# Kernel tuning notes

Measured on AMD Instinct MI355X. Metric: run time of the kernel, lower is better.

Reference implementation:

```python
import jax, jax.numpy as jnp
import numpy as np

N, L, H, D = 8, 1024, 16, 64
HD = H * D          # hidden_size = 1024
MLP = 4 * HD        # mlp_dim = 4096
EPS = 1e-5


def _layer_norm(x, g, b):
    mu = jnp.mean(x, axis=-1, keepdims=True)
    var = jnp.var(x, axis=-1, keepdims=True)
    return (x - mu) * jax.lax.rsqrt(var + EPS) * g + b


def setup_inputs() -> dict:
    key = jax.random.key(0)
    ks = jax.random.split(key, 8)
    s_in = 1.0 / np.sqrt(HD)
    s_mlp = 1.0 / np.sqrt(MLP)
    return {
        "x": jax.random.normal(ks[0], (N, L, HD), jnp.float32),
        "ln0_g": jnp.ones((HD,), jnp.float32),
        "ln0_b": jnp.zeros((HD,), jnp.float32),
        "wq": jax.random.normal(ks[1], (HD, HD), jnp.float32) * s_in,
        "bq": jnp.zeros((HD,), jnp.float32),
        "wk": jax.random.normal(ks[2], (HD, HD), jnp.float32) * s_in,
        "bk": jnp.zeros((HD,), jnp.float32),
        "wv": jax.random.normal(ks[3], (HD, HD), jnp.float32) * s_in,
        "bv": jnp.zeros((HD,), jnp.float32),
        "wo": jax.random.normal(ks[4], (HD, HD), jnp.float32) * s_in,
        "bo": jnp.zeros((HD,), jnp.float32),
        "ln1_g": jnp.ones((HD,), jnp.float32),
        "ln1_b": jnp.zeros((HD,), jnp.float32),
        "w1": jax.random.normal(ks[5], (HD, MLP), jnp.float32) * s_in,
        "b1": jnp.zeros((MLP,), jnp.float32),
        "w2": jax.random.normal(ks[6], (MLP, HD), jnp.float32) * s_mlp,
        "b2": jnp.zeros((HD,), jnp.float32),
    }


def reference(x, ln0_g, ln0_b, wq, bq, wk, bk, wv, bv, wo, bo,
              ln1_g, ln1_b, w1, b1, w2, b2):
    n, l, hd = x.shape
    # --- pre-LN self-attention ---
    y = _layer_norm(x, ln0_g, ln0_b)
    q = (y @ wq + bq).reshape(n, l, H, D)
    k = (y @ wk + bk).reshape(n, l, H, D)
    v = (y @ wv + bv).reshape(n, l, H, D)
    qkt = jnp.einsum('nqhd,nkhd->nqkh', q, k) / jnp.sqrt(jnp.float32(D))
    attn = jax.nn.softmax(qkt, axis=2)
    y = jnp.einsum('nqkh,nkhd->nqhd', attn, v).reshape(n, l, hd)
    y = y @ wo + bo
    x = x + y  # residual (dropout_rate=0 in eval)
    # --- pre-LN MLP ---
    y = _layer_norm(x, ln1_g, ln1_b)
    y = jax.nn.gelu(y @ w1 + b1)
    y = y @ w2 + b2
    return x + y
```

## Files before the change

kernel.cpp:

```cpp
#include <hip/hip_runtime.h>
#include <math.h>

typedef __attribute__((ext_vector_type(8))) __bf16 bf16x8;
typedef __attribute__((ext_vector_type(4))) float f32x4;

#define NBATCH 8
#define SEQ    1024
#define NHEAD  16
#define DHEAD  64
#define HID    1024
#define MLPD   4096

static __device__ __forceinline__ unsigned short f2bf(float f) {
  unsigned int u = __float_as_uint(f);
  u += 0x7fffu + ((u >> 16) & 1u);
  return (unsigned short)(u >> 16);
}

static __device__ __forceinline__ void gload_lds16(const unsigned short* g,
                                                   unsigned short* l) {
  __builtin_amdgcn_global_load_lds(
      (const __attribute__((address_space(1))) unsigned int*)g,
      (__attribute__((address_space(3))) unsigned int*)l, 16, 0, 0);
}

static __device__ __forceinline__ float gelu_fast(float v) {
  const float z = 0.7978845608028654f * (v + 0.044715f * v * v * v);
  const float e = __expf(-2.0f * fabsf(z));
  float th = (1.0f - e) / (1.0f + e);
  th = copysignf(th, z);
  return 0.5f * v * (1.0f + th);
}

__global__ __launch_bounds__(256) void k_transpose(const float* __restrict__ in,
                                                   unsigned short* __restrict__ out,
                                                   int R, int C) {
  __shared__ float t[32][33];
  const int tx = threadIdx.x & 31, ty = threadIdx.x >> 5;
  const int c0 = blockIdx.x * 32, r0 = blockIdx.y * 32;
#pragma unroll
  for (int j = 0; j < 4; ++j)
    t[ty + j * 8][tx] = in[(size_t)(r0 + ty + j * 8) * C + c0 + tx];
  __syncthreads();
#pragma unroll
  for (int j = 0; j < 4; ++j)
    out[(size_t)(c0 + ty + j * 8) * R + r0 + tx] = f2bf(t[tx][ty + j * 8]);
}

__global__ void k_pack_bias(const float* __restrict__ bq, const float* __restrict__ bk,
                            const float* __restrict__ bv, float* __restrict__ o) {
  int i = blockIdx.x * 256 + threadIdx.x;
  if (i < 3 * HID) {
    float v = (i < HID) ? bq[i] : (i < 2 * HID ? bk[i - HID] : bv[i - 2 * HID]);
    o[i] = v;
  }
}

__global__ __launch_bounds__(256) void k_ln(const float* __restrict__ x,
                                            const float* __restrict__ gw,
                                            const float* __restrict__ bw,
                                            unsigned short* __restrict__ y) {
  __shared__ float red[2][4];
  const int row = blockIdx.x;
  const int tid = threadIdx.x;
  const float4 v = ((const float4*)(x + (size_t)row * HID))[tid];
  float sum = v.x + v.y + v.z + v.w;
  float sq  = v.x * v.x + v.y * v.y + v.z * v.z + v.w * v.w;
#pragma unroll
  for (int off = 32; off >= 1; off >>= 1) {
    sum += __shfl_xor(sum, off);
    sq  += __shfl_xor(sq, off);
  }
  if ((tid & 63) == 0) { red[0][tid >> 6] = sum; red[1][tid >> 6] = sq; }
  __syncthreads();
  sum = red[0][0] + red[0][1] + red[0][2] + red[0][3];
  sq  = red[1][0] + red[1][1] + red[1][2] + red[1][3];
  const float mu  = sum * (1.0f / HID);
  const float var = sq * (1.0f / HID) - mu * mu;
  const float rs  = rsqrtf(var + 1e-5f);
  const float4 g4 = ((const float4*)gw)[tid];
  const float4 b4 = ((const float4*)bw)[tid];
  ushort4 ov;
  ov.x = f2bf((v.x - mu) * rs * g4.x + b4.x);
  ov.y = f2bf((v.y - mu) * rs * g4.y + b4.y);
  ov.z = f2bf((v.z - mu) * rs * g4.z + b4.z);
  ov.w = f2bf((v.w - mu) * rs * g4.w + b4.w);
  ((ushort4*)(y + (size_t)row * HID))[tid] = ov;
}

template <int EPI, int BN>
__global__ __launch_bounds__(512, 2) void k_gemm(const unsigned short* __restrict__ A,
                                                 const unsigned short* __restrict__ BT,
                                                 const float* __restrict__ bias,
                                                 const float* __restrict__ res,
                                                 void* __restrict__ Cout,
                                                 int M, int N, int K) {
  constexpr int ASZ = 256 * 64;
  constexpr int BSZ = BN * 64;
  constexpr int NF  = BN / 64;
  constexpr int NCW = BN / 4;
  constexpr int BCALLS = BN / 64;
  __shared__ unsigned short sh[2 * ASZ + 2 * BSZ];

  const int tid  = threadIdx.x;
  const int lane = tid & 63;
  const int w    = tid >> 6;
  const int wr   = w >> 2, wc = w & 3;
  const int l15  = lane & 15, g = lane >> 4;
  const int m0 = blockIdx.y * 256, n0 = blockIdx.x * BN;

  f32x4 acc[8][NF] = {};

  const int srow  = w * 8 + (lane >> 3);
  const int scolb = ((lane & 7) * 16) ^ (((lane >> 3) & 7) << 4);
  const unsigned short* pA = A  + (size_t)(m0 + srow) * K + (scolb >> 1);
  const unsigned short* pB = BT + (size_t)(n0 + srow) * K + (scolb >> 1);
  unsigned short* shB = sh + 2 * ASZ;

#define STAGE(buf, kk)                                                          \
  do {                                                                          \
    _Pragma("unroll") for (int c = 0; c < 4; ++c)                               \
      gload_lds16(pA + (size_t)c * 64 * K + (kk),                               \
                  sh + (buf) * ASZ + (c * 64 + w * 8) * 64);                    \
    _Pragma("unroll") for (int c = 0; c < BCALLS; ++c)                          \
      gload_lds16(pB + (size_t)c * 64 * K + (kk),                               \
                  shB + (buf) * BSZ + (c * 64 + w * 8) * 64);                   \
  } while (0)

  const int fmask = (l15 & 7) << 4;
  const int bo0 = ((0 * 64) + g * 16) ^ fmask;
  const int bo1 = ((1 * 64) + g * 16) ^ fmask;
  const int aRowBase = wr * 128 + l15;
  const int bRowBase = wc * NCW + l15;

  const int NT = K >> 6;

  STAGE(0, 0);
  int buf = 0;
  for (int t = 0; t < NT; ++t) {
    asm volatile("s_waitcnt vmcnt(0)" ::: "memory");
    __builtin_amdgcn_sched_barrier(0);
    __builtin_amdgcn_s_barrier();
    if (t + 1 < NT) STAGE(buf ^ 1, (t + 1) * 64);

    const unsigned short* shAb = sh + buf * ASZ;
    const unsigned short* shBb = shB + buf * BSZ;

    bf16x8 bfr[NF][2];
#pragma unroll
    for (int n = 0; n < NF; ++n) {
      const int br = (bRowBase + n * 16) * 64;
      bfr[n][0] = *(const bf16x8*)(shBb + br + (bo0 >> 1));
      bfr[n][1] = *(const bf16x8*)(shBb + br + (bo1 >> 1));
    }

#pragma unroll
    for (int p = 0; p < 4; ++p) {
      const int ar0 = (aRowBase + (2 * p) * 16) * 64;
      const int ar1 = (aRowBase + (2 * p + 1) * 16) * 64;
      const bf16x8 a00 = *(const bf16x8*)(shAb + ar0 + (bo0 >> 1));
      const bf16x8 a01 = *(const bf16x8*)(shAb + ar0 + (bo1 >> 1));
      const bf16x8 a10 = *(const bf16x8*)(shAb + ar1 + (bo0 >> 1));
      const bf16x8 a11 = *(const bf16x8*)(shAb + ar1 + (bo1 >> 1));
      __builtin_amdgcn_s_barrier();
      asm volatile("s_waitcnt lgkmcnt(0)" ::: "memory");
      __builtin_amdgcn_sched_barrier(0);
      __builtin_amdgcn_s_setprio(1);
#pragma unroll
      for (int n = 0; n < NF; ++n) {
        acc[2 * p][n]     = __builtin_amdgcn_mfma_f32_16x16x32_bf16(a00, bfr[n][0], acc[2 * p][n], 0, 0, 0);
        acc[2 * p][n]     = __builtin_amdgcn_mfma_f32_16x16x32_bf16(a01, bfr[n][1], acc[2 * p][n], 0, 0, 0);
        acc[2 * p + 1][n] = __builtin_amdgcn_mfma_f32_16x16x32_bf16(a10, bfr[n][0], acc[2 * p + 1][n], 0, 0, 0);
        acc[2 * p + 1][n] = __builtin_amdgcn_mfma_f32_16x16x32_bf16(a11, bfr[n][1], acc[2 * p + 1][n], 0, 0, 0);
      }
      __builtin_amdgcn_s_setprio(0);
      __builtin_amdgcn_s_barrier();
    }
    buf ^= 1;
  }
#undef STAGE

  if constexpr (EPI == 2) {
#pragma unroll
    for (int m = 0; m < 8; ++m) {
#pragma unroll
      for (int n = 0; n < NF; ++n) {
        const int col = n0 + wc * NCW + n * 16 + l15;
        const float bc = bias[col];
#pragma unroll
        for (int r = 0; r < 4; ++r) {
          const int row = m0 + wr * 128 + m * 16 + g * 4 + r;
          const size_t idx = (size_t)row * N + col;
          ((float*)Cout)[idx] = acc[m][n][r] + bc + res[idx];
        }
      }
    }
  } else {
    unsigned short* ep = sh + w * (128 * NCW);
#pragma unroll
    for (int m = 0; m < 8; ++m) {
#pragma unroll
      for (int n = 0; n < NF; ++n) {
        const float bc = bias[n0 + wc * NCW + n * 16 + l15];
#pragma unroll
        for (int r = 0; r < 4; ++r) {
          float v = acc[m][n][r] + bc;
          if constexpr (EPI == 1) v = gelu_fast(v);
          ep[(m * 16 + g * 4 + r) * NCW + n * 16 + l15] = f2bf(v);
        }
      }
    }
    constexpr int CPR = NCW / 8;
#pragma unroll
    for (int j = 0; j < NCW / 4; ++j) {
      const int t = lane + j * 64;
      const int row = t / CPR, colb = (t % CPR) * 8;
      const uint4 vv = *(const uint4*)(ep + row * NCW + colb);
      unsigned short* outp = (unsigned short*)Cout +
          (size_t)(m0 + wr * 128 + row) * N + n0 + wc * NCW + colb;
      *(uint4*)outp = vv;
    }
  }
}

__global__ __launch_bounds__(256) void k_vt(const unsigned short* __restrict__ qkv,
                                            unsigned short* __restrict__ vT) {
  __shared__ unsigned short t[64][72];
  const int nh = blockIdx.y;
  const int nb = nh >> 4, h = nh & 15;
  const int l0 = blockIdx.x * 64;
  const int tx = threadIdx.x & 7;
  const int ty = threadIdx.x >> 3;
  const unsigned short* src = qkv + (size_t)(nb * SEQ + l0) * 3072 + 2048 + h * DHEAD;
#pragma unroll
  for (int j = 0; j < 2; ++j)
    *(uint4*)(&t[ty + j * 32][tx * 8]) =
        *(const uint4*)(&src[(size_t)(ty + j * 32) * 3072 + tx * 8]);
  __syncthreads();
  unsigned short* dst = vT + (size_t)nh * DHEAD * SEQ + l0;
#pragma unroll
  for (int j = 0; j < 2; ++j) {
    const int d = ty + j * 32;
    ushort4 a, b;
    a.x = t[tx * 8 + 0][d]; a.y = t[tx * 8 + 1][d];
    a.z = t[tx * 8 + 2][d]; a.w = t[tx * 8 + 3][d];
    b.x = t[tx * 8 + 4][d]; b.y = t[tx * 8 + 5][d];
    b.z = t[tx * 8 + 6][d]; b.w = t[tx * 8 + 7][d];
    *(ushort4*)(&dst[(size_t)d * SEQ + tx * 8])     = a;
    *(ushort4*)(&dst[(size_t)d * SEQ + tx * 8 + 4]) = b;
  }
}

#define SOFTMAX_GROUP(S, gq)                                                       \
  {                                                                                \
    float mx = -INFINITY;                                                          \
    _Pragma("unroll") for (int c = 0; c < 4; ++c)                                  \
      _Pragma("unroll") for (int r = 0; r < 4; ++r)                                \
        mx = fmaxf(mx, S[c][r]);                                                   \
    mx = fmaxf(mx, __shfl_xor(mx, 16));                                            \
    mx = fmaxf(mx, __shfl_xor(mx, 32));                                            \
    const float mnew = fmaxf(m_run[gq], mx);                                       \
    const float sc = __expf(0.125f * (m_run[gq] - mnew));                          \
    m_run[gq] = mnew;                                                              \
    float ts = 0.0f;                                                               \
    _Pragma("unroll") for (int c = 0; c < 4; ++c) {                                \
      const float p0 = __expf(0.125f * (S[c][0] - mnew));                          \
      const float p1 = __expf(0.125f * (S[c][1] - mnew));                          \
      const float p2 = __expf(0.125f * (S[c][2] - mnew));                          \
      const float p3 = __expf(0.125f * (S[c][3] - mnew));                          \
      ts += (p0 + p1) + (p2 + p3);                                                 \
      const unsigned int lo = (unsigned int)f2bf(p0) | ((unsigned int)f2bf(p1) << 16); \
      const unsigned int hi = (unsigned int)f2bf(p2) | ((unsigned int)f2bf(p3) << 16); \
      *(uint2*)(&P_lds[w][((gq) * 16 + l15) * 72 + c * 16 + g * 4]) = make_uint2(lo, hi); \
    }                                                                              \
    ts += __shfl_xor(ts, 16);                                                      \
    ts += __shfl_xor(ts, 32);                                                      \
    s_run[gq] = s_run[gq] * sc + ts;                                               \
    const float scr0 = __shfl(sc, g * 4 + 0), scr1 = __shfl(sc, g * 4 + 1);        \
    const float scr2 = __shfl(sc, g * 4 + 2), scr3 = __shfl(sc, g * 4 + 3);        \
    _Pragma("unroll") for (int dt = 0; dt < 4; ++dt) {                             \
      o[gq][dt][0] *= scr0; o[gq][dt][1] *= scr1;                                  \
      o[gq][dt][2] *= scr2; o[gq][dt][3] *= scr3;                                  \
    }                                                                              \
  }

__global__ __launch_bounds__(256, 4) void k_attn(const unsigned short* __restrict__ qkv,
                                                 const unsigned short* __restrict__ vT,
                                                 unsigned short* __restrict__ outp) {
  __shared__ unsigned short Ks[64 * 64];
  __shared__ unsigned short Vs[64 * 64];
  __shared__ unsigned short P_lds[4][32 * 72];
  const int tid  = threadIdx.x;
  const int lane = tid & 63;
  const int w    = tid >> 6;
  const int l15  = lane & 15, g = lane >> 4;
  const int nh = blockIdx.y;
  const int nb = nh >> 4, h = nh & 15;
  const int q0 = blockIdx.x * 128 + w * 32;
  const size_t RS = 3 * HID;

  const unsigned short* Qp = qkv + (size_t)(nb * SEQ + q0) * RS + h * DHEAD;
  const unsigned short* Kg = qkv + (size_t)(nb * SEQ) * RS + HID + h * DHEAD;
  const unsigned short* Vg = vT + (size_t)nh * DHEAD * SEQ;

  const int L0 = tid * 32, L1 = L0 + 16;
  const int kr0 = L0 >> 7, kc0 = (L0 & 127) ^ ((kr0 & 7) << 4);
  const int kr1 = L1 >> 7, kc1 = (L1 & 127) ^ ((kr1 & 7) << 4);

  bf16x8 aq[2][2];
#pragma unroll
  for (int gq = 0; gq < 2; ++gq)
#pragma unroll
    for (int t = 0; t < 2; ++t)
      aq[gq][t] = *(const bf16x8*)(&Qp[(size_t)(gq * 16 + l15) * RS + t * 32 + g * 8]);

  f32x4 o[2][4] = {};
  float m_run[2] = {-INFINITY, -INFINITY};
  float s_run[2] = {0.0f, 0.0f};

  uint4 rk0, rk1, rv0, rv1;
  rk0 = *(const uint4*)(Kg + (size_t)kr0 * RS + (kc0 >> 1));
  rk1 = *(const uint4*)(Kg + (size_t)kr1 * RS + (kc1 >> 1));
  rv0 = *(const uint4*)(Vg + (size_t)kr0 * SEQ + (kc0 >> 1));
  rv1 = *(const uint4*)(Vg + (size_t)kr1 * SEQ + (kc1 >> 1));
  *(uint4*)(&Ks[tid * 16])     = rk0;
  *(uint4*)(&Ks[tid * 16 + 8]) = rk1;
  *(uint4*)(&Vs[tid * 16])     = rv0;
  *(uint4*)(&Vs[tid * 16 + 8]) = rv1;
  __syncthreads();

  const int sw = (l15 & 7) << 4;

  for (int t16 = 0; t16 < 16; ++t16) {
    if (t16 < 15) {
      const int kb = (t16 + 1) * 64;
      rk0 = *(const uint4*)(Kg + (size_t)(kb + kr0) * RS + (kc0 >> 1));
      rk1 = *(const uint4*)(Kg + (size_t)(kb + kr1) * RS + (kc1 >> 1));
      rv0 = *(const uint4*)(Vg + (size_t)kr0 * SEQ + kb + (kc0 >> 1));
      rv1 = *(const uint4*)(Vg + (size_t)kr1 * SEQ + kb + (kc1 >> 1));
    }

    f32x4 S0[4], S1[4];
#pragma unroll
    for (int c = 0; c < 4; ++c) {
      const int krow = c * 16 + l15;
      const bf16x8 k0 = *(const bf16x8*)(&Ks[krow * 64 + ((( 0 + g * 16) ^ sw) >> 1)]);
      const bf16x8 k1 = *(const bf16x8*)(&Ks[krow * 64 + (((64 + g * 16) ^ sw) >> 1)]);
      f32x4 a = {};
      a = __builtin_amdgcn_mfma_f32_16x16x32_bf16(k0, aq[0][0], a, 0, 0, 0);
      a = __builtin_amdgcn_mfma_f32_16x16x32_bf16(k1, aq[0][1], a, 0, 0, 0);
      S0[c] = a;
      f32x4 b = {};
      b = __builtin_amdgcn_mfma_f32_16x16x32_bf16(k0, aq[1][0], b, 0, 0, 0);
      b = __builtin_amdgcn_mfma_f32_16x16x32_bf16(k1, aq[1][1], b, 0, 0, 0);
      S1[c] = b;
    }

    SOFTMAX_GROUP(S0, 0)
    SOFTMAX_GROUP(S1, 1)

    bf16x8 pa[2][2];
#pragma unroll
    for (int gq = 0; gq < 2; ++gq)
#pragma unroll
      for (int th = 0; th < 2; ++th)
        pa[gq][th] = *(const bf16x8*)(&P_lds[w][(gq * 16 + l15) * 72 + th * 32 + g * 8]);
#pragma unroll
    for (int dt = 0; dt < 4; ++dt) {
      const int vrow = dt * 16 + l15;
      const bf16x8 v0 = *(const bf16x8*)(&Vs[vrow * 64 + ((( 0 + g * 16) ^ sw) >> 1)]);
      const bf16x8 v1 = *(const bf16x8*)(&Vs[vrow * 64 + (((64 + g * 16) ^ sw) >> 1)]);
      o[0][dt] = __builtin_amdgcn_mfma_f32_16x16x32_bf16(pa[0][0], v0, o[0][dt], 0, 0, 0);
      o[0][dt] = __builtin_amdgcn_mfma_f32_16x16x32_bf16(pa[0][1], v1, o[0][dt], 0, 0, 0);
      o[1][dt] = __builtin_amdgcn_mfma_f32_16x16x32_bf16(pa[1][0], v0, o[1][dt], 0, 0, 0);
      o[1][dt] = __builtin_amdgcn_mfma_f32_16x16x32_bf16(pa[1][1], v1, o[1][dt], 0, 0, 0);
    }
    __syncthreads();
    if (t16 < 15) {
      *(uint4*)(&Ks[tid * 16])     = rk0;
      *(uint4*)(&Ks[tid * 16 + 8]) = rk1;
      *(uint4*)(&Vs[tid * 16])     = rv0;
      *(uint4*)(&Vs[tid * 16 + 8]) = rv1;
      __syncthreads();
    }
  }

#pragma unroll
  for (int gq = 0; gq < 2; ++gq) {
    float sr[4];
#pragma unroll
    for (int r = 0; r < 4; ++r) sr[r] = 1.0f / __shfl(s_run[gq], g * 4 + r);
#pragma unroll
    for (int dt = 0; dt < 4; ++dt)
#pragma unroll
      for (int r = 0; r < 4; ++r)
        outp[(size_t)(nb * SEQ + q0 + gq * 16 + g * 4 + r) * HID + h * DHEAD + dt * 16 + l15] =
            f2bf(o[gq][dt][r] * sr[r]);
  }
}

extern "C" void kernel_launch(void* const* d_in, const int* in_sizes, int n_in,
                              void* d_out, int out_size, void* d_ws, size_t ws_size,
                              hipStream_t stream) {
  const float* x    = (const float*)d_in[0];
  const float* ln0g = (const float*)d_in[1];
  const float* ln0b = (const float*)d_in[2];
  const float* wq   = (const float*)d_in[3];
  const float* bq   = (const float*)d_in[4];
  const float* wk   = (const float*)d_in[5];
  const float* bk   = (const float*)d_in[6];
  const float* wv   = (const float*)d_in[7];
  const float* bv   = (const float*)d_in[8];
  const float* wo   = (const float*)d_in[9];
  const float* bo   = (const float*)d_in[10];
  const float* ln1g = (const float*)d_in[11];
  const float* ln1b = (const float*)d_in[12];
  const float* w1   = (const float*)d_in[13];
  const float* b1   = (const float*)d_in[14];
  const float* w2   = (const float*)d_in[15];
  const float* b2   = (const float*)d_in[16];
  float* out = (float*)d_out;

  char* ws = (char*)d_ws;
  unsigned short* qkvT = (unsigned short*)(ws + 0);
  unsigned short* woT  = (unsigned short*)(ws + 6291456);
  unsigned short* w1T  = (unsigned short*)(ws + 8388608);
  unsigned short* w2T  = (unsigned short*)(ws + 16777216);
  float*          bqkv = (float*)(ws + 25165824);
  unsigned short* ybuf = (unsigned short*)(ws + 25178112);
  unsigned short* qkv  = (unsigned short*)(ws + 41955328);
  unsigned short* att  = (unsigned short*)(ws + 92286976);
  unsigned short* hbuf = qkv;
  unsigned short* vT   = ybuf;

  const int M = NBATCH * SEQ;

  k_transpose<<<dim3(32, 32),  256, 0, stream>>>(wq, qkvT,                        HID,  HID);
  k_transpose<<<dim3(32, 32),  256, 0, stream>>>(wk, qkvT + (size_t)1024 * HID,   HID,  HID);
  k_transpose<<<dim3(32, 32),  256, 0, stream>>>(wv, qkvT + (size_t)2048 * HID,   HID,  HID);
  k_transpose<<<dim3(32, 32),  256, 0, stream>>>(wo, woT,                         HID,  HID);
  k_transpose<<<dim3(128, 32), 256, 0, stream>>>(w1, w1T,                         HID,  MLPD);
  k_transpose<<<dim3(32, 128), 256, 0, stream>>>(w2, w2T,                         MLPD, HID);
  k_pack_bias<<<dim3(12), 256, 0, stream>>>(bq, bk, bv, bqkv);

  k_ln<<<dim3(M), 256, 0, stream>>>(x, ln0g, ln0b, ybuf);
  k_gemm<0, 128><<<dim3(24, 32), 512, 0, stream>>>(ybuf, qkvT, bqkv, nullptr, (void*)qkv, M, 3 * HID, HID);
  k_vt<<<dim3(16, 128), 256, 0, stream>>>(qkv, vT);
  k_attn<<<dim3(8, 128), 256, 0, stream>>>(qkv, vT, att);
  k_gemm<2, 128><<<dim3(8, 32), 512, 0, stream>>>(att, woT, bo, x, (void*)out, M, HID, HID);
  k_ln<<<dim3(M), 256, 0, stream>>>(out, ln1g, ln1b, ybuf);
  k_gemm<1, 256><<<dim3(16, 32), 512, 0, stream>>>(ybuf, w1T, b1, nullptr, (void*)hbuf, M, MLPD, HID);
  k_gemm<2, 128><<<dim3(8, 32), 512, 0, stream>>>(hbuf, w2T, b2, out, (void*)out, M, HID, MLPD);
}
```

Before: 399.3 us.

## Interleave next-tile global-to-LDS loads across MFMA phases with partial vmcnt waits

Restructures the GEMM main loop so that prefetches for the next K tile are issued in pieces between the four MFMA phases, instead of all at once at the start of the iteration. Partial s_waitcnt vmcnt counts let B and A chunks arrive in order while earlier chunks are consumed. Several inter-phase barriers are removed, and one barrier is added before the epilogue so the LDS buffer can be reused safely. The aim is to spread memory issue across compute and cut stalls, at the cost of fragile vmcnt accounting that depends on the exact load ordering.

New measurement: 396.9 us. No clear change (-0.6%).

```diff
diff --git a/kernel.cpp b/kernel.cpp
--- a/kernel.cpp
+++ b/kernel.cpp
@@ -31,6 +31,8 @@
   th = copysignf(th, z);
   return 0.5f * v * (1.0f + th);
 }
+
+#define MFMA16(a, b, c) __builtin_amdgcn_mfma_f32_16x16x32_bf16(a, b, c, 0, 0, 0)
 
 __global__ __launch_bounds__(256) void k_transpose(const float* __restrict__ in,
                                                    unsigned short* __restrict__ out,
@@ -99,7 +101,6 @@
   constexpr int BSZ = BN * 64;
   constexpr int NF  = BN / 64;
   constexpr int NCW = BN / 4;
-  constexpr int BCALLS = BN / 64;
   __shared__ unsigned short sh[2 * ASZ + 2 * BSZ];
 
   const int tid  = threadIdx.x;
@@ -117,15 +118,10 @@
   const unsigned short* pB = BT + (size_t)(n0 + srow) * K + (scolb >> 1);
   unsigned short* shB = sh + 2 * ASZ;
 
-#define STAGE(buf, kk)                                                          \
-  do {                                                                          \
-    _Pragma("unroll") for (int c = 0; c < 4; ++c)                               \
-      gload_lds16(pA + (size_t)c * 64 * K + (kk),                               \
-                  sh + (buf) * ASZ + (c * 64 + w * 8) * 64);                    \
-    _Pragma("unroll") for (int c = 0; c < BCALLS; ++c)                          \
-      gload_lds16(pB + (size_t)c * 64 * K + (kk),                               \
-                  shB + (buf) * BSZ + (c * 64 + w * 8) * 64);                   \
-  } while (0)
+#define SB(i, bufv, kk) gload_lds16(pB + (size_t)(i) * 64 * K + (kk), \
+                                    shB + (bufv) * BSZ + ((i) * 64 + w * 8) * 64);
+#define SA(i, bufv, kk) gload_lds16(pA + (size_t)(i) * 64 * K + (kk), \
+                                    sh + (bufv) * ASZ + ((i) * 64 + w * 8) * 64);
 
   const int fmask = (l15 & 7) << 4;
   const int bo0 = ((0 * 64) + g * 16) ^ fmask;
@@ -135,50 +131,75 @@
 
   const int NT = K >> 6;
 
-  STAGE(0, 0);
+  SB(0, 0, 0) SB(1, 0, 0)
+  if constexpr (BN == 256) { SB(2, 0, 0) SB(3, 0, 0) }
+  SA(0, 0, 0) SA(2, 0, 0) SA(1, 0, 0) SA(3, 0, 0)
+
+#define PHASE_TAIL(p, STAGECODE)                                                 \
+  {                                                                              \
+    const int ar0 = (aRowBase + (2 * (p)) * 16) * 64;                            \
+    const int ar1 = (aRowBase + (2 * (p) + 1) * 16) * 64;                        \
+    const bf16x8 a00 = *(const bf16x8*)(shAb + ar0 + (bo0 >> 1));                \
+    const bf16x8 a01 = *(const bf16x8*)(shAb + ar0 + (bo1 >> 1));                \
+    const bf16x8 a10 = *(const bf16x8*)(shAb + ar1 + (bo0 >> 1));                \
+    const bf16x8 a11 = *(const bf16x8*)(shAb + ar1 + (bo1 >> 1));                \
+    STAGECODE                                                                    \
+    __builtin_amdgcn_s_barrier();                                                \
+    asm volatile("s_waitcnt lgkmcnt(0)" ::: "memory");                           \
+    __builtin_amdgcn_sched_barrier(0);                                           \
+    __builtin_amdgcn_s_setprio(1);                                               \
+    _Pragma("unroll") for (int n = 0; n < NF; ++n) {                             \
+      acc[2 * (p)][n]     = MFMA16(a00, bfr[n][0], acc[2 * (p)][n]);             \
+      acc[2 * (p)][n]     = MFMA16(a01, bfr[n][1], acc[2 * (p)][n]);             \
+      acc[2 * (p) + 1][n] = MFMA16(a10, bfr[n][0], acc[2 * (p) + 1][n]);         \
+      acc[2 * (p) + 1][n] = MFMA16(a11, bfr[n][1], acc[2 * (p) + 1][n]);         \
+    }                                                                            \
+    __builtin_amdgcn_s_setprio(0);                                               \
+  }
+
   int buf = 0;
   for (int t = 0; t < NT; ++t) {
-    asm volatile("s_waitcnt vmcnt(0)" ::: "memory");
+    const unsigned short* shAb = sh + buf * ASZ;
+    const unsigned short* shBb = shB + buf * BSZ;
+    const int bufn = buf ^ 1;
+    const int nxt = (t + 1) * 64;
+    const bool more = (t + 1 < NT);
+    bf16x8 bfr[NF][2];
+
+    asm volatile("s_waitcnt vmcnt(2)" ::: "memory");
     __builtin_amdgcn_sched_barrier(0);
     __builtin_amdgcn_s_barrier();
-    if (t + 1 < NT) STAGE(buf ^ 1, (t + 1) * 64);
-
-    const unsigned short* shAb = sh + buf * ASZ;
-    const unsigned short* shBb = shB + buf * BSZ;
-
-    bf16x8 bfr[NF][2];
 #pragma unroll
     for (int n = 0; n < NF; ++n) {
       const int br = (bRowBase + n * 16) * 64;
       bfr[n][0] = *(const bf16x8*)(shBb + br + (bo0 >> 1));
       bfr[n][1] = *(const bf16x8*)(shBb + br + (bo1 >> 1));
     }
-
-#pragma unroll
-    for (int p = 0; p < 4; ++p) {
-      const int ar0 = (aRowBase + (2 * p) * 16) * 64;
-      const int ar1 = (aRowBase + (2 * p + 1) * 16) * 64;
-      const bf16x8 a00 = *(const bf16x8*)(shAb + ar0 + (bo0 >> 1));
-      const bf16x8 a01 = *(const bf16x8*)(shAb + ar0 + (bo1 >> 1));
-      const bf16x8 a10 = *(const bf16x8*)(shAb + ar1 + (bo0 >> 1));
-      const bf16x8 a11 = *(const bf16x8*)(shAb + ar1 + (bo1 >> 1));
-      __builtin_amdgcn_s_barrier();
-      asm volatile("s_waitcnt lgkmcnt(0)" ::: "memory");
-      __builtin_amdgcn_sched_barrier(0);
-      __builtin_amdgcn_s_setprio(1);
-#pragma unroll
-      for (int n = 0; n < NF; ++n) {
-        acc[2 * p][n]     = __builtin_amdgcn_mfma_f32_16x16x32_bf16(a00, bfr[n][0], acc[2 * p][n], 0, 0, 0);
-        acc[2 * p][n]     = __builtin_amdgcn_mfma_f32_16x16x32_bf16(a01, bfr[n][1], acc[2 * p][n], 0, 0, 0);
-        acc[2 * p + 1][n] = __builtin_amdgcn_mfma_f32_16x16x32_bf16(a10, bfr[n][0], acc[2 * p + 1][n], 0, 0, 0);
-        acc[2 * p + 1][n] = __builtin_amdgcn_mfma_f32_16x16x32_bf16(a11, bfr[n][1], acc[2 * p + 1][n], 0, 0, 0);
-      }
-      __builtin_amdgcn_s_setprio(0);
-      __builtin_amdgcn_s_barrier();
-    }
+    PHASE_TAIL(0, if (more) { SB(0, bufn, nxt) SB(1, bufn, nxt) })
+
+    PHASE_TAIL(1, if (more) {
+      if constexpr (BN == 256) { SB(2, bufn, nxt) SB(3, bufn, nxt) }
+      else                     { SA(0, bufn, nxt) SA(2, bufn, nxt) }
+    })
+
+    if (more) asm volatile("s_waitcnt vmcnt(4)" ::: "memory");
+    else      asm volatile("s_waitcnt vmcnt(0)" ::: "memory");
+    __builtin_amdgcn_sched_barrier(0);
+    __builtin_amdgcn_s_barrier();
+    PHASE_TAIL(2, if (more) {
+      if constexpr (BN == 256) { SA(0, bufn, nxt) SA(2, bufn, nxt) }
+      else                     { SA(1, bufn, nxt) SA(3, bufn, nxt) }
+    })
+
+    PHASE_TAIL(3, if (more) {
+      if constexpr (BN == 256) { SA(1, bufn, nxt) SA(3, bufn, nxt) }
+    })
+
     buf ^= 1;
   }
-#undef STAGE
+#undef PHASE_TAIL
+#undef SB
+#undef SA
 
   if constexpr (EPI == 2) {
 #pragma unroll
@@ -196,6 +217,7 @@
       }
     }
   } else {
+    __builtin_amdgcn_s_barrier();
     unsigned short* ep = sh + w * (128 * NCW);
 #pragma unroll
     for (int m = 0; m < 8; ++m) {
@@ -347,12 +369,12 @@
       const bf16x8 k0 = *(const bf16x8*)(&Ks[krow * 64 + ((( 0 + g * 16) ^ sw) >> 1)]);
       const bf16x8 k1 = *(const bf16x8*)(&Ks[krow * 64 + (((64 + g * 16) ^ sw) >> 1)]);
       f32x4 a = {};
-      a = __builtin_amdgcn_mfma_f32_16x16x32_bf16(k0, aq[0][0], a, 0, 0, 0);
-      a = __builtin_amdgcn_mfma_f32_16x16x32_bf16(k1, aq[0][1], a, 0, 0, 0);
+      a = MFMA16(k0, aq[0][0], a);
+      a = MFMA16(k1, aq[0][1], a);
       S0[c] = a;
       f32x4 b = {};
-      b = __builtin_amdgcn_mfma_f32_16x16x32_bf16(k0, aq[1][0], b, 0, 0, 0);
-      b = __builtin_amdgcn_mfma_f32_16x16x32_bf16(k1, aq[1][1], b, 0, 0, 0);
+      b = MFMA16(k0, aq[1][0], b);
+      b = MFMA16(k1, aq[1][1], b);
       S1[c] = b;
     }
 
@@ -370,10 +392,10 @@
       const int vrow = dt * 16 + l15;
       const bf16x8 v0 = *(const bf16x8*)(&Vs[vrow * 64 + ((( 0 + g * 16) ^ sw) >> 1)]);
       const bf16x8 v1 = *(const bf16x8*)(&Vs[vrow * 64 + (((64 + g * 16) ^ sw) >> 1)]);
-      o[0][dt] = __builtin_amdgcn_mfma_f32_16x16x32_bf16(pa[0][0], v0, o[0][dt], 0, 0, 0);
-      o[0][dt] = __builtin_amdgcn_mfma_f32_16x16x32_bf16(pa[0][1], v1, o[0][dt], 0, 0, 0);
-      o[1][dt] = __builtin_amdgcn_mfma_f32_16x16x32_bf16(pa[1][0], v0, o[1][dt], 0, 0, 0);
-      o[1][dt] = __builtin_amdgcn_mfma_f32_16x16x32_bf16(pa[1][1], v1, o[1][dt], 0, 0, 0);
+      o[0][dt] = MFMA16(pa[0][0], v0, o[0][dt]);
+      o[0][dt] = MFMA16(pa[0][1], v1, o[0][dt]);
+      o[1][dt] = MFMA16(pa[1][0], v0, o[1][dt]);
+      o[1][dt] = MFMA16(pa[1][1], v1, o[1][dt]);
     }
     __syncthreads();
     if (t16 < 15) {
```

## Hoist A-fragment LDS loads, drop per-slice barriers, and swizzle GEMM blocks across XCDs

Applied to the files above, without the earlier changes.

In the GEMM main loop, all A fragments for the K-tile are now loaded from LDS up front, before any MFMA work. This removes the two workgroup barriers and the lgkmcnt wait that previously sat inside each of the four MFMA sub-steps, and a barrier is added before the epilogue reuses shared memory. Block IDs are also remapped so that consecutive tiles are spread across the 8 XCDs, aiming for better L2 locality. The cost is higher VGPR pressure from holding 16 A fragments at once, and the remap assumes the grid size is divisible by 8.

After: 376.8 us. 1.06x faster.

```diff
diff --git a/kernel.cpp b/kernel.cpp
--- a/kernel.cpp
+++ b/kernel.cpp
@@ -31,6 +31,8 @@
   th = copysignf(th, z);
   return 0.5f * v * (1.0f + th);
 }
+
+#define MFMA16(a, b, c) __builtin_amdgcn_mfma_f32_16x16x32_bf16(a, b, c, 0, 0, 0)
 
 __global__ __launch_bounds__(256) void k_transpose(const float* __restrict__ in,
                                                    unsigned short* __restrict__ out,
@@ -99,7 +101,6 @@
   constexpr int BSZ = BN * 64;
   constexpr int NF  = BN / 64;
   constexpr int NCW = BN / 4;
-  constexpr int BCALLS = BN / 64;
   __shared__ unsigned short sh[2 * ASZ + 2 * BSZ];
 
   const int tid  = threadIdx.x;
@@ -107,7 +108,12 @@
   const int w    = tid >> 6;
   const int wr   = w >> 2, wc = w & 3;
   const int l15  = lane & 15, g = lane >> 4;
-  const int m0 = blockIdx.y * 256, n0 = blockIdx.x * BN;
+
+  const int gx = gridDim.x;
+  const int nwg = gx * gridDim.y;
+  int lid = blockIdx.y * gx + blockIdx.x;
+  lid = (lid & 7) * (nwg >> 3) + (lid >> 3);
+  const int m0 = (lid / gx) * 256, n0 = (lid % gx) * BN;
 
   f32x4 acc[8][NF] = {};
 
@@ -117,14 +123,14 @@
   const unsigned short* pB = BT + (size_t)(n0 + srow) * K + (scolb >> 1);
   unsigned short* shB = sh + 2 * ASZ;
 
-#define STAGE(buf, kk)                                                          \
-  do {                                                                          \
-    _Pragma("unroll") for (int c = 0; c < 4; ++c)                               \
-      gload_lds16(pA + (size_t)c * 64 * K + (kk),                               \
-                  sh + (buf) * ASZ + (c * 64 + w * 8) * 64);                    \
-    _Pragma("unroll") for (int c = 0; c < BCALLS; ++c)                          \
-      gload_lds16(pB + (size_t)c * 64 * K + (kk),                               \
-                  shB + (buf) * BSZ + (c * 64 + w * 8) * 64);                   \
+#define STAGE(buf_, kk)                                                     \
+  do {                                                                      \
+    _Pragma("unroll") for (int c = 0; c < 4; ++c)                           \
+      gload_lds16(pA + (size_t)c * 64 * K + (kk),                           \
+                  sh + (buf_) * ASZ + (c * 64 + w * 8) * 64);               \
+    _Pragma("unroll") for (int c = 0; c < BN / 64; ++c)                     \
+      gload_lds16(pB + (size_t)c * 64 * K + (kk),                           \
+                  shB + (buf_) * BSZ + (c * 64 + w * 8) * 64);              \
   } while (0)
 
   const int fmask = (l15 & 7) << 4;
@@ -138,14 +144,14 @@
   STAGE(0, 0);
   int buf = 0;
   for (int t = 0; t < NT; ++t) {
+    const unsigned short* shAb = sh + buf * ASZ;
+    const unsigned short* shBb = shB + buf * BSZ;
+
     asm volatile("s_waitcnt vmcnt(0)" ::: "memory");
     __builtin_amdgcn_sched_barrier(0);
     __builtin_amdgcn_s_barrier();
     if (t + 1 < NT) STAGE(buf ^ 1, (t + 1) * 64);
 
-    const unsigned short* shAb = sh + buf * ASZ;
-    const unsigned short* shBb = shB + buf * BSZ;
-
     bf16x8 bfr[NF][2];
 #pragma unroll
     for (int n = 0; n < NF; ++n) {
@@ -153,28 +159,26 @@
       bfr[n][0] = *(const bf16x8*)(shBb + br + (bo0 >> 1));
       bfr[n][1] = *(const bf16x8*)(shBb + br + (bo1 >> 1));
     }
+    bf16x8 afr[8][2];
+#pragma unroll
+    for (int m = 0; m < 8; ++m) {
+      const int ar = (aRowBase + m * 16) * 64;
+      afr[m][0] = *(const bf16x8*)(shAb + ar + (bo0 >> 1));
+      afr[m][1] = *(const bf16x8*)(shAb + ar + (bo1 >> 1));
+    }
+    __builtin_amdgcn_sched_barrier(0);
 
 #pragma unroll
     for (int p = 0; p < 4; ++p) {
-      const int ar0 = (aRowBase + (2 * p) * 16) * 64;
-      const int ar1 = (aRowBase + (2 * p + 1) * 16) * 64;
-      const bf16x8 a00 = *(const bf16x8*)(shAb + ar0 + (bo0 >> 1));
-      const bf16x8 a01 = *(const bf16x8*)(shAb + ar0 + (bo1 >> 1));
-      const bf16x8 a10 = *(const bf16x8*)(shAb + ar1 + (bo0 >> 1));
-      const bf16x8 a11 = *(const bf16x8*)(shAb + ar1 + (bo1 >> 1));
-      __builtin_amdgcn_s_barrier();
-      asm volatile("s_waitcnt lgkmcnt(0)" ::: "memory");
-      __builtin_amdgcn_sched_barrier(0);
       __builtin_amdgcn_s_setprio(1);
 #pragma unroll
       for (int n = 0; n < NF; ++n) {
-        acc[2 * p][n]     = __builtin_amdgcn_mfma_f32_16x16x32_bf16(a00, bfr[n][0], acc[2 * p][n], 0, 0, 0);
-        acc[2 * p][n]     = __builtin_amdgcn_mfma_f32_16x16x32_bf16(a01, bfr[n][1], acc[2 * p][n], 0, 0, 0);
-        acc[2 * p + 1][n] = __builtin_amdgcn_mfma_f32_16x16x32_bf16(a10, bfr[n][0], acc[2 * p + 1][n], 0, 0, 0);
-        acc[2 * p + 1][n] = __builtin_amdgcn_mfma_f32_16x16x32_bf16(a11, bfr[n][1], acc[2 * p + 1][n], 0, 0, 0);
+        acc[2 * p][n]     = MFMA16(afr[2 * p][0],     bfr[n][0], acc[2 * p][n]);
+        acc[2 * p][n]     = MFMA16(afr[2 * p][1],     bfr[n][1], acc[2 * p][n]);
+        acc[2 * p + 1][n] = MFMA16(afr[2 * p + 1][0], bfr[n][0], acc[2 * p + 1][n]);
+        acc[2 * p + 1][n] = MFMA16(afr[2 * p + 1][1], bfr[n][1], acc[2 * p + 1][n]);
       }
       __builtin_amdgcn_s_setprio(0);
-      __builtin_amdgcn_s_barrier();
     }
     buf ^= 1;
   }
@@ -196,6 +200,7 @@
       }
     }
   } else {
+    __builtin_amdgcn_s_barrier();
     unsigned short* ep = sh + w * (128 * NCW);
 #pragma unroll
     for (int m = 0; m < 8; ++m) {
@@ -347,12 +352,12 @@
       const bf16x8 k0 = *(const bf16x8*)(&Ks[krow * 64 + ((( 0 + g * 16) ^ sw) >> 1)]);
       const bf16x8 k1 = *(const bf16x8*)(&Ks[krow * 64 + (((64 + g * 16) ^ sw) >> 1)]);
       f32x4 a = {};
-      a = __builtin_amdgcn_mfma_f32_16x16x32_bf16(k0, aq[0][0], a, 0, 0, 0);
-      a = __builtin_amdgcn_mfma_f32_16x16x32_bf16(k1, aq[0][1], a, 0, 0, 0);
+      a = MFMA16(k0, aq[0][0], a);
+      a = MFMA16(k1, aq[0][1], a);
       S0[c] = a;
       f32x4 b = {};
-      b = __builtin_amdgcn_mfma_f32_16x16x32_bf16(k0, aq[1][0], b, 0, 0, 0);
-      b = __builtin_amdgcn_mfma_f32_16x16x32_bf16(k1, aq[1][1], b, 0, 0, 0);
+      b = MFMA16(k0, aq[1][0], b);
+      b = MFMA16(k1, aq[1][1], b);
       S1[c] = b;
     }
 
@@ -370,10 +375,10 @@
       const int vrow = dt * 16 + l15;
       const bf16x8 v0 = *(const bf16x8*)(&Vs[vrow * 64 + ((( 0 + g * 16) ^ sw) >> 1)]);
       const bf16x8 v1 = *(const bf16x8*)(&Vs[vrow * 64 + (((64 + g * 16) ^ sw) >> 1)]);
-      o[0][dt] = __builtin_amdgcn_mfma_f32_16x16x32_bf16(pa[0][0], v0, o[0][dt], 0, 0, 0);
-      o[0][dt] = __builtin_amdgcn_mfma_f32_16x16x32_bf16(pa[0][1], v1, o[0][dt], 0, 0, 0);
-      o[1][dt] = __builtin_amdgcn_mfma_f32_16x16x32_bf16(pa[1][0], v0, o[1][dt], 0, 0, 0);
-      o[1][dt] = __builtin_amdgcn_mfma_f32_16x16x32_bf16(pa[1][1], v1, o[1][dt], 0, 0, 0);
+      o[0][dt] = MFMA16(pa[0][0], v0, o[0][dt]);
+      o[0][dt] = MFMA16(pa[0][1], v1, o[0][dt]);
+      o[1][dt] = MFMA16(pa[1][0], v0, o[1][dt]);
+      o[1][dt] = MFMA16(pa[1][1], v1, o[1][dt]);
     }
     __syncthreads();
     if (t16 < 15) {
```
